# Kernel optimization log

Hardware: AMD Instinct MI355X
Metric: run time of the kernel (lower is better)

The kernel has to match this reference:

```python
import jax, jax.numpy as jnp
import numpy as np


def _bitrev_indices(N):
    # bit-reversal permutation, vectorized in numpy (static, N known at trace time)
    bits = int(np.log2(N))
    idx = np.arange(N, dtype=np.int64)
    rev = np.zeros(N, dtype=np.int64)
    for _ in range(bits):
        rev = (rev << 1) | (idx & 1)
        idx >>= 1
    return jnp.asarray(rev)


def setup_inputs() -> dict:
    key = jax.random.key(0)
    k1, k2 = jax.random.split(key)
    B, N = 2048, 4096
    return {
        "x_re": jax.random.normal(k1, (B, N), dtype=jnp.float32),
        "x_im": jax.random.normal(k2, (B, N), dtype=jnp.float32),
    }


def reference(x_re, x_im):
    # Radix-2 decimation-in-time Cooley-Tukey FFT, faithful to PythonFFT.forward
    N = x_re.shape[-1]
    batch = x_re.shape[:-1]
    num_stages = int(np.log2(N))

    # twiddle table W_N^k = exp(-2*pi*i*k/N) (matches compute_twiddle_table)
    k = jnp.arange(N, dtype=jnp.float32)
    angles = (-2.0 * np.pi) * k / N
    W_re_tab = jnp.cos(angles)
    W_im_tab = jnp.sin(angles)

    br = _bitrev_indices(N)
    y_re = x_re[..., br]
    y_im = x_im[..., br]

    # loop over log2(N) stages (small fixed loop); each stage is fully vectorized
    for stage in range(num_stages):
        stride = 1 << stage
        group = stride << 1
        # twiddle index for butterfly position j in a group: j * (N // group) % N
        tw_idx = (jnp.arange(stride) * (N // group)) % N
        w_re = W_re_tab[tw_idx]  # [stride]
        w_im = W_im_tab[tw_idx]  # [stride]

        yr = y_re.reshape(*batch, N // group, 2, stride)
        yi = y_im.reshape(*batch, N // group, 2, stride)
        a_re, b_re = yr[..., 0, :], yr[..., 1, :]
        a_im, b_im = yi[..., 0, :], yi[..., 1, :]

        wb_re = w_re * b_re - w_im * b_im
        wb_im = w_re * b_im + w_im * b_re

        y_re = jnp.stack([a_re + wb_re, a_re - wb_re], axis=-2).reshape(*batch, N)
        y_im = jnp.stack([a_im + wb_im, a_im - wb_im], axis=-2).reshape(*batch, N)

    return (y_re, y_im)
```

## Files before the change

kernel.cpp:

```cpp
#include <hip/hip_runtime.h>
#include <math.h>

#define FFT_N   4096
#define THREADS 256
#define RH 0.70710678118654752f
#define C16 0.92387953251128676f
#define S16 0.38268343236508977f
#define NEG2PI_256  (-2.45436926061702597e-2f)
#define NEG2PI_4096 (-1.53398078788564123e-3f)

#define POS(k) ((((k) & 3) << 2) | ((k) >> 2))

__device__ __forceinline__ float2 cmul(float2 a, float2 b) {
    return make_float2(a.x * b.x - a.y * b.y, a.x * b.y + a.y * b.x);
}

__device__ __forceinline__ void dft4(float2& a, float2& b, float2& c, float2& d) {
    float2 t0 = make_float2(a.x + c.x, a.y + c.y);
    float2 t1 = make_float2(a.x - c.x, a.y - c.y);
    float2 t2 = make_float2(b.x + d.x, b.y + d.y);
    float2 t3 = make_float2(b.y - d.y, d.x - b.x);
    a = make_float2(t0.x + t2.x, t0.y + t2.y);
    b = make_float2(t1.x + t3.x, t1.y + t3.y);
    c = make_float2(t0.x - t2.x, t0.y - t2.y);
    d = make_float2(t1.x - t3.x, t1.y - t3.y);
}

template<int E>
__device__ __forceinline__ float2 mw16(float2 z) {
    if constexpr (E == 0) return z;
    else if constexpr (E == 4) return make_float2(z.y, -z.x);
    else if constexpr (E == 2) return make_float2(RH * (z.x + z.y), RH * (z.y - z.x));
    else if constexpr (E == 6) return make_float2(RH * (z.y - z.x), -RH * (z.x + z.y));
    else if constexpr (E == 1) return cmul(z, make_float2(C16, -S16));
    else if constexpr (E == 3) return cmul(z, make_float2(S16, -C16));
    else           return cmul(z, make_float2(-C16, S16));
}

__device__ __forceinline__ void dft16(float2 (&v)[16]) {
    dft4(v[0], v[4], v[8],  v[12]);
    dft4(v[1], v[5], v[9],  v[13]);
    dft4(v[2], v[6], v[10], v[14]);
    dft4(v[3], v[7], v[11], v[15]);
    v[5]  = mw16<1>(v[5]);   v[9]  = mw16<2>(v[9]);   v[13] = mw16<3>(v[13]);
    v[6]  = mw16<2>(v[6]);   v[10] = mw16<4>(v[10]);  v[14] = mw16<6>(v[14]);
    v[7]  = mw16<3>(v[7]);   v[11] = mw16<6>(v[11]);  v[15] = mw16<9>(v[15]);
    dft4(v[0],  v[1],  v[2],  v[3]);
    dft4(v[4],  v[5],  v[6],  v[7]);
    dft4(v[8],  v[9],  v[10], v[11]);
    dft4(v[12], v[13], v[14], v[15]);
}

__global__ __launch_bounds__(THREADS)
void fft4096_r16(const float* __restrict__ xre, const float* __restrict__ xim,
                 float* __restrict__ yre, float* __restrict__ yim)
{
    __shared__ float2 sd[FFT_N];

    const int t  = threadIdx.x;
    const int lo = t & 15;
    const int hi = t >> 4;
    const size_t off = (size_t)blockIdx.x * FFT_N;
    const float* xr = xre + off;
    const float* xi = xim + off;

    float2 v[16];
    #pragma unroll
    for (int n3 = 0; n3 < 16; ++n3) {
        v[n3].x = xr[t + (n3 << 8)];
        v[n3].y = xi[t + (n3 << 8)];
    }
    dft16(v);

    {
        float sn, cs;
        __sincosf((float)hi * NEG2PI_256, &sn, &cs);
        float2 b[4], c[4];
        b[0] = make_float2(1.f, 0.f);
        b[1] = make_float2(cs, sn);
        b[2] = cmul(b[1], b[1]);
        b[3] = cmul(b[2], b[1]);
        c[0] = make_float2(1.f, 0.f);
        c[1] = cmul(b[2], b[2]);
        c[2] = cmul(c[1], c[1]);
        c[3] = cmul(c[2], c[1]);
        #pragma unroll
        for (int k3 = 0; k3 < 16; ++k3) {
            float2 z = v[POS(k3)];
            if (k3 & 3)  z = cmul(z, b[k3 & 3]);
            if (k3 >> 2) z = cmul(z, c[k3 >> 2]);
            sd[t + (k3 << 8)] = z;
        }
    }
    __syncthreads();

    #pragma unroll
    for (int n2 = 0; n2 < 16; ++n2)
        v[n2] = sd[lo + (n2 << 4) + (hi << 8)];
    __syncthreads();

    dft16(v);

    {
        float sn, cs;
        __sincosf((float)(lo * hi) * NEG2PI_4096, &sn, &cs);
        const float2 P = make_float2(cs, sn);
        __sincosf((float)lo * NEG2PI_256, &sn, &cs);
        float2 w1 = make_float2(cs, sn);
        float2 w2 = cmul(w1, w1);
        float2 w3 = cmul(w2, w1);
        float2 Pw[4], z[4];
        Pw[0] = P;
        Pw[1] = cmul(P, w1);
        Pw[2] = cmul(P, w2);
        Pw[3] = cmul(P, w3);
        z[0] = make_float2(1.f, 0.f);
        z[1] = cmul(w2, w2);
        z[2] = cmul(z[1], z[1]);
        z[3] = cmul(z[2], z[1]);
        const int wb = (hi ^ lo) + (lo << 8);
        #pragma unroll
        for (int k2 = 0; k2 < 16; ++k2) {
            float2 u = cmul(v[POS(k2)], Pw[k2 & 3]);
            if (k2 >> 2) u = cmul(u, z[k2 >> 2]);
            sd[wb + (k2 << 4)] = u;
        }
    }
    __syncthreads();

    #pragma unroll
    for (int m = 0; m < 16; ++m)
        v[m] = sd[(lo ^ m) + (hi << 4) + (m << 8)];

    dft16(v);
    float* yr = yre + off;
    float* yi = yim + off;
    #pragma unroll
    for (int k1 = 0; k1 < 16; ++k1) {
        __builtin_nontemporal_store(v[POS(k1)].x, &yr[t + (k1 << 8)]);
        __builtin_nontemporal_store(v[POS(k1)].y, &yi[t + (k1 << 8)]);
    }
}

extern "C" void kernel_launch(void* const* d_in, const int* in_sizes, int n_in,
                              void* d_out, int out_size, void* d_ws, size_t ws_size,
                              hipStream_t stream) {
    const float* xre = (const float*)d_in[0];
    const float* xim = (const float*)d_in[1];
    const int total = in_sizes[0];
    const int rows  = total / FFT_N;
    float* yre = (float*)d_out;
    float* yim = yre + total;
    fft4096_r16<<<dim3(rows), dim3(THREADS), 0, stream>>>(xre, xim, yre, yim);
}
```

Before: 27.29 us.

## Process two FFT rows per block with prefetched second row and lighter barriers

Each block now handles two rows. It issues the global loads for both rows up front so the second row's loads overlap the first row's compute. __syncthreads is replaced by an explicit LDS waitcnt plus s_barrier, which avoids waiting on outstanding global memory ops. The cost is twice the registers for input data, which may reduce occupancy, and half as many blocks. The grid assumes an even row count.

```diff
diff --git a/kernel.cpp b/kernel.cpp
--- a/kernel.cpp
+++ b/kernel.cpp
@@ -13,6 +13,11 @@
 
 __device__ __forceinline__ float2 cmul(float2 a, float2 b) {
     return make_float2(a.x * b.x - a.y * b.y, a.x * b.y + a.y * b.x);
+}
+
+__device__ __forceinline__ void bar_lds() {
+    asm volatile("s_waitcnt lgkmcnt(0)" ::: "memory");
+    __builtin_amdgcn_s_barrier();
 }
 
 __device__ __forceinline__ void dft4(float2& a, float2& b, float2& c, float2& d) {
@@ -51,25 +56,20 @@
     dft4(v[12], v[13], v[14], v[15]);
 }
 
-__global__ __launch_bounds__(THREADS)
-void fft4096_r16(const float* __restrict__ xre, const float* __restrict__ xim,
-                 float* __restrict__ yre, float* __restrict__ yim)
-{
-    __shared__ float2 sd[FFT_N];
-
-    const int t  = threadIdx.x;
-    const int lo = t & 15;
-    const int hi = t >> 4;
-    const size_t off = (size_t)blockIdx.x * FFT_N;
-    const float* xr = xre + off;
-    const float* xi = xim + off;
-
-    float2 v[16];
+__device__ __forceinline__ void load_row(float2 (&v)[16],
+                                         const float* __restrict__ xr,
+                                         const float* __restrict__ xi, int t) {
     #pragma unroll
     for (int n3 = 0; n3 < 16; ++n3) {
         v[n3].x = xr[t + (n3 << 8)];
         v[n3].y = xi[t + (n3 << 8)];
     }
+}
+
+__device__ __forceinline__ void process_row(float2 (&v)[16], float2* __restrict__ sd,
+                                            int t, int lo, int hi,
+                                            float* __restrict__ yr,
+                                            float* __restrict__ yi) {
     dft16(v);
 
     {
@@ -92,12 +92,12 @@
             sd[t + (k3 << 8)] = z;
         }
     }
-    __syncthreads();
+    bar_lds();
 
     #pragma unroll
     for (int n2 = 0; n2 < 16; ++n2)
         v[n2] = sd[lo + (n2 << 4) + (hi << 8)];
-    __syncthreads();
+    bar_lds();
 
     dft16(v);
 
@@ -126,20 +126,39 @@
             sd[wb + (k2 << 4)] = u;
         }
     }
-    __syncthreads();
+    bar_lds();
 
     #pragma unroll
     for (int m = 0; m < 16; ++m)
         v[m] = sd[(lo ^ m) + (hi << 4) + (m << 8)];
 
     dft16(v);
-    float* yr = yre + off;
-    float* yi = yim + off;
     #pragma unroll
     for (int k1 = 0; k1 < 16; ++k1) {
         __builtin_nontemporal_store(v[POS(k1)].x, &yr[t + (k1 << 8)]);
         __builtin_nontemporal_store(v[POS(k1)].y, &yi[t + (k1 << 8)]);
     }
+}
+
+__global__ __launch_bounds__(THREADS)
+void fft4096_r16p(const float* __restrict__ xre, const float* __restrict__ xim,
+                  float* __restrict__ yre, float* __restrict__ yim)
+{
+    __shared__ float2 sd[FFT_N];
+
+    const int t  = threadIdx.x;
+    const int lo = t & 15;
+    const int hi = t >> 4;
+    const size_t off0 = (size_t)(2 * blockIdx.x) * FFT_N;
+    const size_t off1 = off0 + FFT_N;
+
+    float2 va[16], vb[16];
+    load_row(va, xre + off0, xim + off0, t);
+    load_row(vb, xre + off1, xim + off1, t);
+
+    process_row(va, sd, t, lo, hi, yre + off0, yim + off0);
+    bar_lds();
+    process_row(vb, sd, t, lo, hi, yre + off1, yim + off1);
 }
 
 extern "C" void kernel_launch(void* const* d_in, const int* in_sizes, int n_in,
@@ -151,5 +170,5 @@
     const int rows  = total / FFT_N;
     float* yre = (float*)d_out;
     float* yim = yre + total;
-    fft4096_r16<<<dim3(rows), dim3(THREADS), 0, stream>>>(xre, xim, yre, yim);
+    fft4096_r16p<<<dim3(rows / 2), dim3(THREADS), 0, stream>>>(xre, xim, yre, yim);
 }
```

New measurement: 26.47 us. 3.0% less time.

## Halve shared memory by exchanging FFT transposes in two half passes

Applied to the files above, without the earlier changes.

Shrinks the LDS buffer from 32KB to 16KB per block. Each transpose exchange is now done in two halves, with the low and high thread halves taking turns writing and reading. Stage 2 and stage 3 use remapped index patterns so that each half fits. The goal is to fit more blocks per CU and better hide global memory latency. The cost is extra barriers and more live registers (separate u/w arrays), which could limit occupancy through VGPR pressure instead.

```diff
diff --git a/kernel.cpp b/kernel.cpp
--- a/kernel.cpp
+++ b/kernel.cpp
@@ -13,6 +13,11 @@
 
 __device__ __forceinline__ float2 cmul(float2 a, float2 b) {
     return make_float2(a.x * b.x - a.y * b.y, a.x * b.y + a.y * b.x);
+}
+
+__device__ __forceinline__ void bar_lds() {
+    asm volatile("s_waitcnt lgkmcnt(0)" ::: "memory");
+    __builtin_amdgcn_s_barrier();
 }
 
 __device__ __forceinline__ void dft4(float2& a, float2& b, float2& c, float2& d) {
@@ -52,14 +57,15 @@
 }
 
 __global__ __launch_bounds__(THREADS)
-void fft4096_r16(const float* __restrict__ xre, const float* __restrict__ xim,
-                 float* __restrict__ yre, float* __restrict__ yim)
+void fft4096_r16c(const float* __restrict__ xre, const float* __restrict__ xim,
+                  float* __restrict__ yre, float* __restrict__ yim)
 {
-    __shared__ float2 sd[FFT_N];
+    __shared__ float2 sd[FFT_N / 2];
 
     const int t  = threadIdx.x;
     const int lo = t & 15;
     const int hi = t >> 4;
+    const bool lowhalf = (hi < 8);
     const size_t off = (size_t)blockIdx.x * FFT_N;
     const float* xr = xre + off;
     const float* xi = xim + off;
@@ -72,10 +78,10 @@
     }
     dft16(v);
 
+    float2 b[4], c[4];
     {
         float sn, cs;
         __sincosf((float)hi * NEG2PI_256, &sn, &cs);
-        float2 b[4], c[4];
         b[0] = make_float2(1.f, 0.f);
         b[1] = make_float2(cs, sn);
         b[2] = cmul(b[1], b[1]);
@@ -84,23 +90,41 @@
         c[1] = cmul(b[2], b[2]);
         c[2] = cmul(c[1], c[1]);
         c[3] = cmul(c[2], c[1]);
+    }
+
+    if (lowhalf) {
         #pragma unroll
         for (int k3 = 0; k3 < 16; ++k3) {
             float2 z = v[POS(k3)];
             if (k3 & 3)  z = cmul(z, b[k3 & 3]);
             if (k3 >> 2) z = cmul(z, c[k3 >> 2]);
-            sd[t + (k3 << 8)] = z;
+            sd[lo + (k3 << 4) + ((hi & 7) << 8)] = z;
         }
     }
-    __syncthreads();
+    bar_lds();
+    float2 u[16];
+    #pragma unroll
+    for (int n2 = 0; n2 < 8; ++n2)
+        u[n2] = sd[t + (n2 << 8)];
+    bar_lds();
+    if (!lowhalf) {
+        #pragma unroll
+        for (int k3 = 0; k3 < 16; ++k3) {
+            float2 z = v[POS(k3)];
+            if (k3 & 3)  z = cmul(z, b[k3 & 3]);
+            if (k3 >> 2) z = cmul(z, c[k3 >> 2]);
+            sd[lo + (k3 << 4) + ((hi & 7) << 8)] = z;
+        }
+    }
+    bar_lds();
+    #pragma unroll
+    for (int n2 = 8; n2 < 16; ++n2)
+        u[n2] = sd[t + ((n2 & 7) << 8)];
+    bar_lds();
 
-    #pragma unroll
-    for (int n2 = 0; n2 < 16; ++n2)
-        v[n2] = sd[lo + (n2 << 4) + (hi << 8)];
-    __syncthreads();
+    dft16(u);
 
-    dft16(v);
-
+    float2 Pw[4], zz[4];
     {
         float sn, cs;
         __sincosf((float)(lo * hi) * NEG2PI_4096, &sn, &cs);
@@ -109,36 +133,51 @@
         float2 w1 = make_float2(cs, sn);
         float2 w2 = cmul(w1, w1);
         float2 w3 = cmul(w2, w1);
-        float2 Pw[4], z[4];
         Pw[0] = P;
         Pw[1] = cmul(P, w1);
         Pw[2] = cmul(P, w2);
         Pw[3] = cmul(P, w3);
-        z[0] = make_float2(1.f, 0.f);
-        z[1] = cmul(w2, w2);
-        z[2] = cmul(z[1], z[1]);
-        z[3] = cmul(z[2], z[1]);
-        const int wb = (hi ^ lo) + (lo << 8);
-        #pragma unroll
-        for (int k2 = 0; k2 < 16; ++k2) {
-            float2 u = cmul(v[POS(k2)], Pw[k2 & 3]);
-            if (k2 >> 2) u = cmul(u, z[k2 >> 2]);
-            sd[wb + (k2 << 4)] = u;
-        }
+        zz[0] = make_float2(1.f, 0.f);
+        zz[1] = cmul(w2, w2);
+        zz[2] = cmul(zz[1], zz[1]);
+        zz[3] = cmul(zz[2], zz[1]);
     }
-    __syncthreads();
+    const int wb2 = (lo ^ hi) + (hi << 4);
 
     #pragma unroll
-    for (int m = 0; m < 16; ++m)
-        v[m] = sd[(lo ^ m) + (hi << 4) + (m << 8)];
+    for (int k2 = 0; k2 < 8; ++k2) {
+        float2 z = cmul(u[POS(k2)], Pw[k2 & 3]);
+        if (k2 >> 2) z = cmul(z, zz[k2 >> 2]);
+        sd[wb2 + (k2 << 8)] = z;
+    }
+    bar_lds();
+    float2 w[16];
+    if (lowhalf) {
+        #pragma unroll
+        for (int m = 0; m < 16; ++m)
+            w[m] = sd[(m ^ lo) + (lo << 4) + ((hi & 7) << 8)];
+    }
+    bar_lds();
+    #pragma unroll
+    for (int k2 = 8; k2 < 16; ++k2) {
+        float2 z = cmul(u[POS(k2)], Pw[k2 & 3]);
+        z = cmul(z, zz[k2 >> 2]);
+        sd[wb2 + ((k2 & 7) << 8)] = z;
+    }
+    bar_lds();
+    if (!lowhalf) {
+        #pragma unroll
+        for (int m = 0; m < 16; ++m)
+            w[m] = sd[(m ^ lo) + (lo << 4) + ((hi & 7) << 8)];
+    }
 
-    dft16(v);
+    dft16(w);
     float* yr = yre + off;
     float* yi = yim + off;
     #pragma unroll
     for (int k1 = 0; k1 < 16; ++k1) {
-        __builtin_nontemporal_store(v[POS(k1)].x, &yr[t + (k1 << 8)]);
-        __builtin_nontemporal_store(v[POS(k1)].y, &yi[t + (k1 << 8)]);
+        __builtin_nontemporal_store(w[POS(k1)].x, &yr[t + (k1 << 8)]);
+        __builtin_nontemporal_store(w[POS(k1)].y, &yi[t + (k1 << 8)]);
     }
 }
 
@@ -151,5 +190,5 @@
     const int rows  = total / FFT_N;
     float* yre = (float*)d_out;
     float* yim = yre + total;
-    fft4096_r16<<<dim3(rows), dim3(THREADS), 0, stream>>>(xre, xim, yre, yim);
+    fft4096_r16c<<<dim3(rows), dim3(THREADS), 0, stream>>>(xre, xim, yre, yim);
 }
```

Measured after the change: 27.21 us. Within noise of the previous version (-0.3%).
